# Performance work log

Hardware: AMD Instinct MI355X
Metric: run time of the kernel (lower is better)

The kernel has to match this reference:

```python
import jax, jax.numpy as jnp
import numpy as np

SR = 48000
HARMONIC_NUM = 8          # -> 9 harmonics total
SINE_AMP = 0.1
NOISE_STD = 0.003
VOICED_THRESHOLD = 0.0
B, T, UPP = 8, 2000, 480
S = T * UPP


def setup_inputs() -> dict:
    key = jax.random.key(0)
    k_f0, k_mask, k_ri, k_noise = jax.random.split(key, 4)
    f0 = jax.random.uniform(k_f0, (B, 1, T), jnp.float32, 80.0, 500.0)
    voiced = (jax.random.uniform(k_mask, (B, 1, T)) > 0.2).astype(jnp.float32)
    f0 = f0 * voiced
    # random initial phases; harmonic 0 gets phase 0 (as in torch code)
    rand_ini = jax.random.uniform(k_ri, (B, HARMONIC_NUM + 1), jnp.float32)
    rand_ini = rand_ini.at[:, 0].set(0.0)
    noise_raw = jax.random.normal(k_noise, (B, S), jnp.float32)
    # linear mixing layer: weight = 1/(H+1), bias = 0 per nn.init in __init__
    w = jnp.full((HARMONIC_NUM + 1,), 1.0 / (HARMONIC_NUM + 1), jnp.float32)
    b = jnp.zeros((1,), jnp.float32)
    return {"f0": f0, "rand_ini": rand_ini, "noise_raw": noise_raw,
            "w": w, "b": b, "upp": UPP}


def reference(f0, rand_ini, noise_raw, w, b, upp):
    # f0: [B,1,T] Hz -> nearest-upsample to [B, S]
    f0u = jnp.repeat(f0[:, 0, :], upp, axis=1)              # [B, S]
    uv = (f0u > VOICED_THRESHOLD).astype(f0.dtype)          # [B, S]
    rad = f0u * (2.0 * np.pi / SR)
    # cumsum is linear: one cumsum, broadcast-multiply by harmonic index
    base_phase = jnp.cumsum(rad, axis=1)                    # [B, S]
    mult = jnp.arange(1, HARMONIC_NUM + 2, dtype=f0.dtype)  # [H+1]
    phase = base_phase[:, :, None] * mult + rand_ini[:, None, :] * (2.0 * np.pi)
    sines = jnp.sin(phase) * uv[:, :, None]                 # [B, S, H+1]
    har = jnp.tanh(sines @ w + b[0]) * SINE_AMP             # [B, S]
    noise = noise_raw * NOISE_STD                            # [B, S]
    return har[:, None, :], noise[:, None, :], uv[:, None, :]
```

## Files before the change

### kernel.cpp

```cpp
#include <hip/hip_runtime.h>
#include <hip/hip_bf16.h>
#include <math.h>

constexpr int   B_   = 8;
constexpr int   T_   = 2000;
constexpr int   UPP_ = 480;
constexpr int   S_   = T_ * UPP_;
constexpr int   NH   = 9;
constexpr float INV_SR = 1.0f / 48000.0f;

constexpr int   BLK  = 320;
constexpr int   J_   = 3;
constexpr int   QPB  = BLK * J_;
constexpr int   SPB  = QPB * 4;
constexpr int   QPR  = S_ / 4;
constexpr int   BPR  = QPR / QPB;

typedef float fx4 __attribute__((ext_vector_type(4)));

#if __has_builtin(__builtin_amdgcn_sinf)
__device__ __forceinline__ float sinrev(float x) { return __builtin_amdgcn_sinf(x); }
#else
__device__ __forceinline__ float sinrev(float x) { return __sinf(x * 6.2831853071795864769f); }
#endif
#if __has_builtin(__builtin_amdgcn_cosf)
__device__ __forceinline__ float cosrev(float x) { return __builtin_amdgcn_cosf(x); }
#else
__device__ __forceinline__ float cosrev(float x) { return __cosf(x * 6.2831853071795864769f); }
#endif

__device__ __forceinline__ fx4 nt_load4(const float* p) {
    return __builtin_nontemporal_load((const fx4*)p);
}
__device__ __forceinline__ void st4(float* p, float a, float b, float c, float d) {
    fx4 v = {a, b, c, d};
    *(fx4*)p = v;
}

__global__ __launch_bounds__(256) void frame_scan_kernel(
    const float* __restrict__ f0,
    const float* __restrict__ rand_ini,
    const float* __restrict__ w,
    float2* __restrict__ ftab,
    float2* __restrict__ abtab)
{
    __shared__ double wsum[4];
    const int b    = blockIdx.x;
    const int j    = threadIdx.x;
    const int lane = j & 63;
    const int wid  = j >> 6;
    constexpr int CH = 8;
    const int t0 = j * CH;

    if (j < NH) {
        float ri = rand_ini[b * NH + j];
        float wv = w[j];
        abtab[b * NH + j] = make_float2(wv * cosrev(ri), wv * sinrev(ri));
    }

    float fc[CH];
    double local = 0.0;
    #pragma unroll
    for (int k = 0; k < CH; ++k) {
        int t = t0 + k;
        float v = (t < T_) ? f0[b * T_ + t] : 0.0f;
        fc[k] = v * INV_SR;
        local += (double)fc[k] * (double)UPP_;
    }

    double x = local;
    #pragma unroll
    for (int off = 1; off < 64; off <<= 1) {
        double y = __shfl_up(x, off, 64);
        if (lane >= off) x += y;
    }
    if (lane == 63) wsum[wid] = x;
    __syncthreads();

    double woff = 0.0;
    #pragma unroll
    for (int ww = 0; ww < 3; ++ww)
        if (ww < wid) woff += wsum[ww];

    double excl = (x + woff) - local;

    #pragma unroll
    for (int k = 0; k < CH; ++k) {
        int t = t0 + k;
        if (t < T_) {
            double ph = excl - floor(excl);
            ftab[b * T_ + t] = make_float2((float)ph, fc[k]);
            excl += (double)fc[k] * (double)UPP_;
        }
    }
}

__global__ __launch_bounds__(BLK) void synth_kernel(
    const float* __restrict__ noise_raw,
    const float* __restrict__ bb,
    const float2* __restrict__ ftab,
    const float2* __restrict__ abtab,
    float* __restrict__ out)
{
    const int bblk = blockIdx.x / BPR;
    const int rblk = blockIdx.x - bblk * BPR;
    const int tid  = threadIdx.x;
    const int qbase = rblk * QPB + tid;

    float A[NH], Bc[NH];
    #pragma unroll
    for (int h = 0; h < NH; ++h) {
        float2 ab = abtab[bblk * NH + h];
        A[h]  = ab.x;
        Bc[h] = ab.y;
    }
    const float bias = bb[0];

    const float* __restrict__ nzr = noise_raw + (size_t)bblk * S_;
    const float2* __restrict__ ftr = ftab + bblk * T_;

    int    s0[J_];
    fx4    nz[J_];
    float2 pf[J_];

    #pragma unroll
    for (int j = 0; j < J_; ++j) {
        int q = qbase + j * BLK;
        s0[j] = q * 4;
        nz[j] = nt_load4(nzr + s0[j]);
    }
    #pragma unroll
    for (int j = 0; j < J_; ++j)
        pf[j] = ftr[s0[j] / UPP_];

    float har[J_][4];
    float uvfv[J_];
    #pragma unroll
    for (int j = 0; j < J_; ++j) {
        const float Pred = pf[j].x;
        const float fcyc = pf[j].y;
        const float uvf  = (fcyc > 0.0f) ? 1.0f : 0.0f;
        uvfv[j] = uvf;
        const int  i0   = s0[j] - (s0[j] / UPP_) * UPP_;
        #pragma unroll
        for (int k = 0; k < 4; ++k) {
            float basef = Pred + fcyc * (float)(i0 + 1 + k);
            float f     = basef - floorf(basef);
            float s1    = sinrev(f);
            float c1    = cosrev(f);
            float tc    = c1 + c1;
            float sm1 = 0.0f, cm1 = 1.0f;
            float sm  = s1,   cm  = c1;
            float acc = 0.0f;
            #pragma unroll
            for (int h = 0; h < NH; ++h) {
                acc = fmaf(sm, A[h], acc);
                acc = fmaf(cm, Bc[h], acc);
                float sn = fmaf(tc, sm, -sm1);
                float cn = fmaf(tc, cm, -cm1);
                sm1 = sm; cm1 = cm; sm = sn; cm = cn;
            }
            float xx = fmaf(acc, uvf, bias);
            float e  = __expf(2.0f * xx);
            har[j][k] = (e - 1.0f) / (e + 1.0f) * 0.1f;
        }
    }

    float* __restrict__ harp = out + (size_t)bblk * S_;
    float* __restrict__ nzp  = harp + (size_t)B_ * S_;
    float* __restrict__ uvp  = harp + (size_t)2 * B_ * S_;

    #pragma unroll
    for (int j = 0; j < J_; ++j) {
        st4(harp + s0[j], har[j][0], har[j][1], har[j][2], har[j][3]);
        st4(nzp + s0[j], nz[j].x * 0.003f, nz[j].y * 0.003f,
                         nz[j].z * 0.003f, nz[j].w * 0.003f);
        st4(uvp + s0[j], uvfv[j], uvfv[j], uvfv[j], uvfv[j]);
    }
}

extern "C" void kernel_launch(void* const* d_in, const int* in_sizes, int n_in,
                              void* d_out, int out_size, void* d_ws, size_t ws_size,
                              hipStream_t stream) {
    const float* f0        = (const float*)d_in[0];
    const float* rand_ini  = (const float*)d_in[1];
    const float* noise_raw = (const float*)d_in[2];
    const float* w         = (const float*)d_in[3];
    const float* bb        = (const float*)d_in[4];

    float2* ftab  = (float2*)d_ws;
    float2* abtab = (float2*)((char*)d_ws + 128000);

    frame_scan_kernel<<<B_, 256, 0, stream>>>(f0, rand_ini, w, ftab, abtab);
    synth_kernel<<<B_ * BPR, BLK, 0, stream>>>(
        noise_raw, bb, ftab, abtab, (float*)d_out);
}
```

Measured before the change: 31.89 us.

## Split synth kernel into role-specialized blocks for harmonic, noise, and uv outputs

Triples the synth grid and gives each block one role: noise scaling, voiced-mask writing, or harmonic synthesis. Before, every block loaded noise, computed sines and wrote all three outputs. The split lets the memory-bound noise and uv blocks run alongside the compute-bound harmonic blocks and shortens each block's live ranges. It adds more block launches and reads the frame table twice.

```diff
diff --git a/kernel.cpp b/kernel.cpp
--- a/kernel.cpp
+++ b/kernel.cpp
@@ -12,9 +12,9 @@
 constexpr int   BLK  = 320;
 constexpr int   J_   = 3;
 constexpr int   QPB  = BLK * J_;
-constexpr int   SPB  = QPB * 4;
 constexpr int   QPR  = S_ / 4;
 constexpr int   BPR  = QPR / QPB;
+constexpr int   NBR  = B_ * BPR;
 
 typedef float fx4 __attribute__((ext_vector_type(4)));
 
@@ -102,10 +102,45 @@
     const float2* __restrict__ abtab,
     float* __restrict__ out)
 {
-    const int bblk = blockIdx.x / BPR;
-    const int rblk = blockIdx.x - bblk * BPR;
+    const int role = blockIdx.x / NBR;
+    const int rr   = blockIdx.x - role * NBR;
+    const int bblk = rr / BPR;
+    const int rblk = rr - bblk * BPR;
     const int tid  = threadIdx.x;
     const int qbase = rblk * QPB + tid;
+
+    const size_t rowoff = (size_t)bblk * S_;
+
+    if (role == 1) {
+        const float* __restrict__ nzr = noise_raw + rowoff;
+        float* __restrict__ nzp = out + (size_t)B_ * S_ + rowoff;
+        fx4 nz[J_];
+        int s0[J_];
+        #pragma unroll
+        for (int j = 0; j < J_; ++j) {
+            s0[j] = (qbase + j * BLK) * 4;
+            nz[j] = nt_load4(nzr + s0[j]);
+        }
+        #pragma unroll
+        for (int j = 0; j < J_; ++j)
+            st4(nzp + s0[j], nz[j].x * 0.003f, nz[j].y * 0.003f,
+                             nz[j].z * 0.003f, nz[j].w * 0.003f);
+        return;
+    }
+
+    const float2* __restrict__ ftr = ftab + bblk * T_;
+
+    if (role == 2) {
+        float* __restrict__ uvp = out + (size_t)2 * B_ * S_ + rowoff;
+        #pragma unroll
+        for (int j = 0; j < J_; ++j) {
+            int s0 = (qbase + j * BLK) * 4;
+            float fcyc = ftr[s0 / UPP_].y;
+            float uvf  = (fcyc > 0.0f) ? 1.0f : 0.0f;
+            st4(uvp + s0, uvf, uvf, uvf, uvf);
+        }
+        return;
+    }
 
     float A[NH], Bc[NH];
     #pragma unroll
@@ -115,33 +150,19 @@
         Bc[h] = ab.y;
     }
     const float bias = bb[0];
-
-    const float* __restrict__ nzr = noise_raw + (size_t)bblk * S_;
-    const float2* __restrict__ ftr = ftab + bblk * T_;
-
-    int    s0[J_];
-    fx4    nz[J_];
-    float2 pf[J_];
+    float* __restrict__ harp = out + rowoff;
 
     #pragma unroll
     for (int j = 0; j < J_; ++j) {
-        int q = qbase + j * BLK;
-        s0[j] = q * 4;
-        nz[j] = nt_load4(nzr + s0[j]);
-    }
-    #pragma unroll
-    for (int j = 0; j < J_; ++j)
-        pf[j] = ftr[s0[j] / UPP_];
-
-    float har[J_][4];
-    float uvfv[J_];
-    #pragma unroll
-    for (int j = 0; j < J_; ++j) {
-        const float Pred = pf[j].x;
-        const float fcyc = pf[j].y;
+        const int   s0   = (qbase + j * BLK) * 4;
+        const int   t    = s0 / UPP_;
+        const int   i0   = s0 - t * UPP_;
+        const float2 pf  = ftr[t];
+        const float Pred = pf.x;
+        const float fcyc = pf.y;
         const float uvf  = (fcyc > 0.0f) ? 1.0f : 0.0f;
-        uvfv[j] = uvf;
-        const int  i0   = s0[j] - (s0[j] / UPP_) * UPP_;
+
+        float har[4];
         #pragma unroll
         for (int k = 0; k < 4; ++k) {
             float basef = Pred + fcyc * (float)(i0 + 1 + k);
@@ -162,20 +183,9 @@
             }
             float xx = fmaf(acc, uvf, bias);
             float e  = __expf(2.0f * xx);
-            har[j][k] = (e - 1.0f) / (e + 1.0f) * 0.1f;
-        }
-    }
-
-    float* __restrict__ harp = out + (size_t)bblk * S_;
-    float* __restrict__ nzp  = harp + (size_t)B_ * S_;
-    float* __restrict__ uvp  = harp + (size_t)2 * B_ * S_;
-
-    #pragma unroll
-    for (int j = 0; j < J_; ++j) {
-        st4(harp + s0[j], har[j][0], har[j][1], har[j][2], har[j][3]);
-        st4(nzp + s0[j], nz[j].x * 0.003f, nz[j].y * 0.003f,
-                         nz[j].z * 0.003f, nz[j].w * 0.003f);
-        st4(uvp + s0[j], uvfv[j], uvfv[j], uvfv[j], uvfv[j]);
+            har[k]   = (e - 1.0f) / (e + 1.0f) * 0.1f;
+        }
+        st4(harp + s0, har[0], har[1], har[2], har[3]);
     }
 }
 
@@ -192,6 +202,6 @@
     float2* abtab = (float2*)((char*)d_ws + 128000);
 
     frame_scan_kernel<<<B_, 256, 0, stream>>>(f0, rand_ini, w, ftab, abtab);
-    synth_kernel<<<B_ * BPR, BLK, 0, stream>>>(
+    synth_kernel<<<3 * NBR, BLK, 0, stream>>>(
         noise_raw, bb, ftab, abtab, (float*)d_out);
 }
```

Measured after the change: 37.14 us. 1.16x slower.
